# Kernel optimization log

Hardware: AMD Instinct MI355X
Metric: run time of the kernel (lower is better)

## Reference

```python
import jax, jax.numpy as jnp
import numpy as np
import math

V_ORDER = 22
N_ORDER = 22
HID = 128
MAX_ABS = 0.99
LOG_F0_MIN = math.log(80.0)
LOG_F0_MAX = math.log(1000.0)
OUT = 1 + V_ORDER + 1 + N_ORDER + 1 + HID  # 175


def setup_inputs() -> dict:
    key = jax.random.key(0)
    k1, k2, k3 = jax.random.split(key, 3)
    B, F, D = 32, 1000, 1024
    h = jax.random.normal(k1, (B, F, D), jnp.float32)
    W = jax.random.normal(k2, (OUT, D), jnp.float32) * 0.02
    b = jax.random.normal(k3, (OUT,), jnp.float32) * 0.1
    return {"h": h, "W": W, "b": b}


def _logits2biquads(logits):
    # conj representation: logits (..., 2) -> monic biquad coeffs (..., 3)
    mag = jax.nn.sigmoid(logits[..., 0]) * MAX_ABS
    phase = jax.nn.sigmoid(logits[..., 1]) * jnp.pi
    a1 = -2.0 * mag * jnp.cos(phase)
    a2 = mag * mag
    return jnp.stack([jnp.ones_like(a1), a1, a2], axis=-1)


def _biquads2lpc(biquads):
    # biquads: (..., S, 3) monic sections -> full LPC poly coeffs (..., 2S)
    # sequentially convolve the S second-order sections (b0 == 1 exactly)
    S = biquads.shape[-2]
    L = 2 * S + 1
    poly = jnp.zeros(biquads.shape[:-2] + (L,), biquads.dtype).at[..., 0].set(1.0)

    def shift(p, n):
        pad = [(0, 0)] * (p.ndim - 1) + [(n, 0)]
        return jnp.pad(p, pad)[..., :L]

    for i in range(S):  # small fixed S (=11), fully vectorized over batch/frames
        a1 = biquads[..., i, 1:2]
        a2 = biquads[..., i, 2:3]
        poly = poly + shift(poly, 1) * a1 + shift(poly, 2) * a2
    return poly[..., 1:]  # drop leading 1


def reference(h, W, b):
    B, F, _ = h.shape
    y = jnp.einsum('bfd,od->bfo', h, W) + b  # backbone out_linear
    idx = np.cumsum([1, V_ORDER, 1, N_ORDER, 1])
    f0_l, v_lpc_l, v_gain_l, n_lpc_l, n_gain_l, h_feat = jnp.split(y, idx, axis=-1)
    f0 = jnp.exp(jax.nn.sigmoid(f0_l[..., 0]) * (LOG_F0_MAX - LOG_F0_MIN) + LOG_F0_MIN)
    voice_lpc = _biquads2lpc(_logits2biquads(v_lpc_l.reshape(B, F, -1, 2)))
    noise_lpc = _biquads2lpc(_logits2biquads(n_lpc_l.reshape(B, F, -1, 2)))
    voice_gain = jnp.exp(v_gain_l[..., 0])
    noise_gain = jnp.exp(n_gain_l[..., 0])
    # flat version of (f0, (h,), (voice_gain, voice_lpc), (noise_gain, noise_lpc), ())
    return (f0, h_feat, voice_gain, voice_lpc, noise_gain, noise_lpc)
```

## Files before the change

### kernel.cpp

```cpp
#include <hip/hip_runtime.h>
#include <math.h>

#define D_DIM  1024
#define OUT_N  175
#define HID_N  128
#define BM     64
#define BK     32
#define NWR    176
#define LDK    40

#define V_OFF   1
#define VG_OFF  23
#define N_OFF   24
#define NG_OFF  46
#define HF_OFF  47

#define LOG_F0_MIN 4.3820266346738812f
#define LOG_F0_MAX 6.9077552789821368f
#define PI_F       3.14159265358979323846f

typedef __attribute__((ext_vector_type(8))) short s16x8;
typedef __attribute__((ext_vector_type(4))) short s16x4;
typedef __attribute__((ext_vector_type(4))) float f32x4;

static __device__ __forceinline__ short f2bf(float f) {
    unsigned u = __float_as_uint(f);
    unsigned r = (u + 0x7fffu + ((u >> 16) & 1u)) >> 16;
    return (short)r;
}
static __device__ __forceinline__ float bf2f(short s) {
    return __uint_as_float(((unsigned)(unsigned short)s) << 16);
}

__global__ __launch_bounds__(256) void split_w_kernel(
    const float* __restrict__ W, short* __restrict__ whi, short* __restrict__ wlo)
{
    const int n = blockIdx.x;
    const int k = threadIdx.x << 2;
    float4 v = make_float4(0.f, 0.f, 0.f, 0.f);
    if (n < OUT_N) v = *(const float4*)(W + (size_t)n * D_DIM + k);
    s16x4 hv, lv;
    hv.x = f2bf(v.x); lv.x = f2bf(v.x - bf2f(hv.x));
    hv.y = f2bf(v.y); lv.y = f2bf(v.y - bf2f(hv.y));
    hv.z = f2bf(v.z); lv.z = f2bf(v.z - bf2f(hv.z));
    hv.w = f2bf(v.w); lv.w = f2bf(v.w - bf2f(hv.w));
    *(s16x4*)(whi + n * D_DIM + k) = hv;
    *(s16x4*)(wlo + n * D_DIM + k) = lv;
}

#define SMEM_BYTES 45312

__global__ __launch_bounds__(256) void glottal_main(
    const float* __restrict__ h, const short* __restrict__ whi,
    const short* __restrict__ wlo, const float* __restrict__ bias,
    float* __restrict__ out, int R)
{
    __shared__ __align__(16) char smem[SMEM_BYTES];
    short* AhiS = (short*)smem;
    short* AloS = AhiS + BM * LDK;
    short* WhiS = AloS + BM * LDK;
    short* WloS = WhiS + NWR * LDK;
    float (*yS)[OUT_N + 2] = (float (*)[OUT_N + 2])smem;

    const int tid = threadIdx.x;
    const int r0  = blockIdx.x * BM;

    const int rA  = tid >> 3;
    const int kqA = (tid & 7) << 2;
    const int rW  = tid >> 2;
    const int kqW = (tid & 3) << 3;

    const int lane = tid & 63;
    const int wid  = tid >> 6;
    const int c    = lane & 15;
    const int kg   = lane >> 4;
    const int jcnt = (wid < 3) ? 3 : 2;
    const int fragOff = c * LDK + kg * 8;

    f32x4 acc[4][3];
    #pragma unroll
    for (int m = 0; m < 4; ++m)
        #pragma unroll
        for (int jj = 0; jj < 3; ++jj) acc[m][jj] = f32x4{0.f, 0.f, 0.f, 0.f};

    float4 apf0, apf1;
    s16x8 wph0, wph1, wph2, wpl0, wpl1, wpl2;

    int gA0 = r0 + rA;      if (gA0 >= R) gA0 = R - 1;
    int gA1 = r0 + rA + 32; if (gA1 >= R) gA1 = R - 1;
    const float* hP0 = h + (size_t)gA0 * D_DIM + kqA;
    const float* hP1 = h + (size_t)gA1 * D_DIM + kqA;
    const int nW0 = rW, nW1 = rW + 64, nW2 = rW + 128;
    const short* wHP = whi + rW * D_DIM + kqW;
    const short* wLP = wlo + rW * D_DIM + kqW;
    const bool w2ok = (nW2 < NWR);

    apf0 = *(const float4*)(hP0);
    apf1 = *(const float4*)(hP1);
    wph0 = *(const s16x8*)(wHP);
    wpl0 = *(const s16x8*)(wLP);
    wph1 = *(const s16x8*)(wHP + 64 * D_DIM);
    wpl1 = *(const s16x8*)(wLP + 64 * D_DIM);
    if (w2ok) { wph2 = *(const s16x8*)(wHP + 128 * D_DIM);
                wpl2 = *(const s16x8*)(wLP + 128 * D_DIM); }

    for (int kt = 0; kt < D_DIM; kt += BK) {
        {
            s16x4 hv, lv;
            hv.x = f2bf(apf0.x); lv.x = f2bf(apf0.x - bf2f(hv.x));
            hv.y = f2bf(apf0.y); lv.y = f2bf(apf0.y - bf2f(hv.y));
            hv.z = f2bf(apf0.z); lv.z = f2bf(apf0.z - bf2f(hv.z));
            hv.w = f2bf(apf0.w); lv.w = f2bf(apf0.w - bf2f(hv.w));
            *(s16x4*)(AhiS + rA * LDK + kqA) = hv;
            *(s16x4*)(AloS + rA * LDK + kqA) = lv;
            hv.x = f2bf(apf1.x); lv.x = f2bf(apf1.x - bf2f(hv.x));
            hv.y = f2bf(apf1.y); lv.y = f2bf(apf1.y - bf2f(hv.y));
            hv.z = f2bf(apf1.z); lv.z = f2bf(apf1.z - bf2f(hv.z));
            hv.w = f2bf(apf1.w); lv.w = f2bf(apf1.w - bf2f(hv.w));
            *(s16x4*)(AhiS + (rA + 32) * LDK + kqA) = hv;
            *(s16x4*)(AloS + (rA + 32) * LDK + kqA) = lv;
            *(s16x8*)(WhiS + nW0 * LDK + kqW) = wph0;
            *(s16x8*)(WloS + nW0 * LDK + kqW) = wpl0;
            *(s16x8*)(WhiS + nW1 * LDK + kqW) = wph1;
            *(s16x8*)(WloS + nW1 * LDK + kqW) = wpl1;
            if (w2ok) {
                *(s16x8*)(WhiS + nW2 * LDK + kqW) = wph2;
                *(s16x8*)(WloS + nW2 * LDK + kqW) = wpl2;
            }
        }
        __syncthreads();

        const int ktn = kt + BK;
        if (ktn < D_DIM) {
            apf0 = *(const float4*)(hP0 + ktn);
            apf1 = *(const float4*)(hP1 + ktn);
            wph0 = *(const s16x8*)(wHP + ktn);
            wpl0 = *(const s16x8*)(wLP + ktn);
            wph1 = *(const s16x8*)(wHP + 64 * D_DIM + ktn);
            wpl1 = *(const s16x8*)(wLP + 64 * D_DIM + ktn);
            if (w2ok) { wph2 = *(const s16x8*)(wHP + 128 * D_DIM + ktn);
                        wpl2 = *(const s16x8*)(wLP + 128 * D_DIM + ktn); }
        }

        s16x8 ahv[4], alv[4];
        #pragma unroll
        for (int m = 0; m < 4; ++m) {
            ahv[m] = *(const s16x8*)(AhiS + (m << 4) * LDK + fragOff);
            alv[m] = *(const s16x8*)(AloS + (m << 4) * LDK + fragOff);
        }
        #pragma unroll
        for (int jj = 0; jj < 3; ++jj) {
            if (jj < jcnt) {
                const int j = wid * 3 + jj;
                s16x8 bh = *(const s16x8*)(WhiS + (j << 4) * LDK + fragOff);
                s16x8 bl = *(const s16x8*)(WloS + (j << 4) * LDK + fragOff);
                #pragma unroll
                for (int m = 0; m < 4; ++m) {
                    acc[m][jj] = __builtin_amdgcn_mfma_f32_16x16x32_bf16(ahv[m], bh, acc[m][jj], 0, 0, 0);
                    acc[m][jj] = __builtin_amdgcn_mfma_f32_16x16x32_bf16(ahv[m], bl, acc[m][jj], 0, 0, 0);
                    acc[m][jj] = __builtin_amdgcn_mfma_f32_16x16x32_bf16(alv[m], bh, acc[m][jj], 0, 0, 0);
                }
            }
        }
        __syncthreads();
    }

    #pragma unroll
    for (int jj = 0; jj < 3; ++jj) {
        if (jj < jcnt) {
            const int j   = wid * 3 + jj;
            const int col = (j << 4) + c;
            if (col < OUT_N) {
                const float bb = bias[col];
                #pragma unroll
                for (int m = 0; m < 4; ++m)
                    #pragma unroll
                    for (int r = 0; r < 4; ++r)
                        yS[(m << 4) + (kg << 2) + r][col] = acc[m][jj][r] + bb;
            }
        }
    }
    __syncthreads();

    const size_t Rz = (size_t)R;

    for (int e = tid; e < BM * HID_N; e += 256) {
        int rr = e >> 7, cc = e & (HID_N - 1);
        int gr = r0 + rr;
        if (gr < R)
            out[Rz + (size_t)gr * HID_N + cc] = yS[rr][HF_OFF + cc];
    }

    if (tid < 2 * BM) {
        const int rr   = tid >> 1;
        const int half = tid & 1;
        const int gr   = r0 + rr;
        if (gr < R) {
            const float* yrow = yS[rr];

            if (half == 0) {
                float s = 1.f / (1.f + expf(-yrow[0]));
                out[gr] = expf(s * (LOG_F0_MAX - LOG_F0_MIN) + LOG_F0_MIN);
            }

            const int lbase = half ? N_OFF  : V_OFF;
            const int gidx  = half ? NG_OFF : VG_OFF;
            float*    gout  = out + (half ? Rz * 152 : Rz * 129);
            float*    lout  = out + (half ? Rz * 153 : Rz * 130);

            gout[gr] = expf(yrow[gidx]);

            float poly[23];
            poly[0] = 1.f;
            #pragma unroll
            for (int j = 1; j < 23; ++j) poly[j] = 0.f;

            #pragma unroll
            for (int i = 0; i < 11; ++i) {
                float l0  = yrow[lbase + 2 * i];
                float l1  = yrow[lbase + 2 * i + 1];
                float mag = 0.99f / (1.f + expf(-l0));
                float ph  = PI_F   / (1.f + expf(-l1));
                float a1  = -2.f * mag * cosf(ph);
                float a2  = mag * mag;
                #pragma unroll
                for (int j = 22; j >= 2; --j)
                    poly[j] = fmaf(a1, poly[j - 1], fmaf(a2, poly[j - 2], poly[j]));
                poly[1] = fmaf(a1, poly[0], poly[1]);
            }

            #pragma unroll
            for (int j = 0; j < 22; ++j)
                lout[(size_t)gr * 22 + j] = poly[j + 1];
        }
    }
}

extern "C" void kernel_launch(void* const* d_in, const int* in_sizes, int n_in,
                              void* d_out, int out_size, void* d_ws, size_t ws_size,
                              hipStream_t stream) {
    const float* h    = (const float*)d_in[0];
    const float* W    = (const float*)d_in[1];
    const float* bias = (const float*)d_in[2];
    float* out        = (float*)d_out;

    const int R = in_sizes[0] / D_DIM;
    const int blocks = (R + BM - 1) / BM;

    short* whi = (short*)d_ws;
    short* wlo = whi + NWR * D_DIM;

    split_w_kernel<<<NWR, 256, 0, stream>>>(W, whi, wlo);
    glottal_main<<<blocks, 256, 0, stream>>>(h, whi, wlo, bias, out, R);
}
```

Baseline: 216.7 us.

## Pre-swizzle W into MFMA fragment layout and load B directly from global

The weight split kernel now writes W hi/lo parts in per-lane MFMA fragment order, so the main kernel reads B operands straight from global/L2 into registers instead of staging them through LDS. The main kernel grows to 512 threads arranged as 2 row-halves by 4 column groups, and LDS shrinks to the A tile only, which should allow higher occupancy and fewer LDS writes and barriers' worth of traffic. The hidden-feature columns are written directly from the accumulators, and only the first 47 columns go through LDS for the LPC epilogue. The risk is that each wave now issues more global loads per k-step, so performance depends on L2 hit rate for W, and the direct hidden-feature stores are less coalesced.

```diff
diff --git a/kernel.cpp b/kernel.cpp
--- a/kernel.cpp
+++ b/kernel.cpp
@@ -6,8 +6,10 @@
 #define HID_N  128
 #define BM     64
 #define BK     32
-#define NWR    176
+#define NT     (D_DIM / BK)
 #define LDK    40
+#define NFRAG  11
+#define FRAG_STRIDE 512
 
 #define V_OFF   1
 #define VG_OFF  23
@@ -32,164 +34,167 @@
     return __uint_as_float(((unsigned)(unsigned short)s) << 16);
 }
 
-__global__ __launch_bounds__(256) void split_w_kernel(
-    const float* __restrict__ W, short* __restrict__ whi, short* __restrict__ wlo)
+__global__ __launch_bounds__(64) void build_wfrag(
+    const float* __restrict__ W, short* __restrict__ whiF, short* __restrict__ wloF)
 {
-    const int n = blockIdx.x;
-    const int k = threadIdx.x << 2;
-    float4 v = make_float4(0.f, 0.f, 0.f, 0.f);
-    if (n < OUT_N) v = *(const float4*)(W + (size_t)n * D_DIM + k);
-    s16x4 hv, lv;
-    hv.x = f2bf(v.x); lv.x = f2bf(v.x - bf2f(hv.x));
-    hv.y = f2bf(v.y); lv.y = f2bf(v.y - bf2f(hv.y));
-    hv.z = f2bf(v.z); lv.z = f2bf(v.z - bf2f(hv.z));
-    hv.w = f2bf(v.w); lv.w = f2bf(v.w - bf2f(hv.w));
-    *(s16x4*)(whi + n * D_DIM + k) = hv;
-    *(s16x4*)(wlo + n * D_DIM + k) = lv;
-}
-
-#define SMEM_BYTES 45312
-
-__global__ __launch_bounds__(256) void glottal_main(
-    const float* __restrict__ h, const short* __restrict__ whi,
-    const short* __restrict__ wlo, const float* __restrict__ bias,
+    const int ft   = blockIdx.x;
+    const int j    = ft >> 5;
+    const int t    = ft & 31;
+    const int lane = threadIdx.x;
+    const int n    = 16 * j + (lane & 15);
+    const int k    = 32 * t + (lane >> 4) * 8;
+
+    float v[8];
+    if (n < OUT_N) {
+        float4 p0 = *(const float4*)(W + (size_t)n * D_DIM + k);
+        float4 p1 = *(const float4*)(W + (size_t)n * D_DIM + k + 4);
+        v[0] = p0.x; v[1] = p0.y; v[2] = p0.z; v[3] = p0.w;
+        v[4] = p1.x; v[5] = p1.y; v[6] = p1.z; v[7] = p1.w;
+    } else {
+        #pragma unroll
+        for (int e = 0; e < 8; ++e) v[e] = 0.f;
+    }
+    s16x8 hv, lv;
+    #pragma unroll
+    for (int e = 0; e < 8; ++e) {
+        short hb = f2bf(v[e]);
+        hv[e] = hb;
+        lv[e] = f2bf(v[e] - bf2f(hb));
+    }
+    const size_t off = ((size_t)ft * 64 + lane) * 8;
+    *(s16x8*)(whiF + off) = hv;
+    *(s16x8*)(wloF + off) = lv;
+}
+
+#define SMEM_BYTES 12544
+
+__global__ __launch_bounds__(512, 4) void glottal_main(
+    const float* __restrict__ h, const short* __restrict__ whiF,
+    const short* __restrict__ wloF, const float* __restrict__ bias,
     float* __restrict__ out, int R)
 {
     __shared__ __align__(16) char smem[SMEM_BYTES];
     short* AhiS = (short*)smem;
     short* AloS = AhiS + BM * LDK;
-    short* WhiS = AloS + BM * LDK;
-    short* WloS = WhiS + NWR * LDK;
-    float (*yS)[OUT_N + 2] = (float (*)[OUT_N + 2])smem;
-
-    const int tid = threadIdx.x;
-    const int r0  = blockIdx.x * BM;
-
-    const int rA  = tid >> 3;
-    const int kqA = (tid & 7) << 2;
-    const int rW  = tid >> 2;
-    const int kqW = (tid & 3) << 3;
+    float (*yS)[49] = (float (*)[49])smem;
+
+    const int tid  = threadIdx.x;
+    const int r0   = blockIdx.x * BM;
 
     const int lane = tid & 63;
     const int wid  = tid >> 6;
     const int c    = lane & 15;
     const int kg   = lane >> 4;
-    const int jcnt = (wid < 3) ? 3 : 2;
-    const int fragOff = c * LDK + kg * 8;
-
-    f32x4 acc[4][3];
-    #pragma unroll
-    for (int m = 0; m < 4; ++m)
-        #pragma unroll
-        for (int jj = 0; jj < 3; ++jj) acc[m][jj] = f32x4{0.f, 0.f, 0.f, 0.f};
-
-    float4 apf0, apf1;
-    s16x8 wph0, wph1, wph2, wpl0, wpl1, wpl2;
-
-    int gA0 = r0 + rA;      if (gA0 >= R) gA0 = R - 1;
-    int gA1 = r0 + rA + 32; if (gA1 >= R) gA1 = R - 1;
-    const float* hP0 = h + (size_t)gA0 * D_DIM + kqA;
-    const float* hP1 = h + (size_t)gA1 * D_DIM + kqA;
-    const int nW0 = rW, nW1 = rW + 64, nW2 = rW + 128;
-    const short* wHP = whi + rW * D_DIM + kqW;
-    const short* wLP = wlo + rW * D_DIM + kqW;
-    const bool w2ok = (nW2 < NWR);
-
-    apf0 = *(const float4*)(hP0);
-    apf1 = *(const float4*)(hP1);
-    wph0 = *(const s16x8*)(wHP);
-    wpl0 = *(const s16x8*)(wLP);
-    wph1 = *(const s16x8*)(wHP + 64 * D_DIM);
-    wpl1 = *(const s16x8*)(wLP + 64 * D_DIM);
-    if (w2ok) { wph2 = *(const s16x8*)(wHP + 128 * D_DIM);
-                wpl2 = *(const s16x8*)(wLP + 128 * D_DIM); }
-
-    for (int kt = 0; kt < D_DIM; kt += BK) {
+    const int mh   = wid >> 2;
+    const int jg   = wid & 3;
+    const int jcnt = (jg < 3) ? 3 : 2;
+
+    const int rA  = tid >> 3;
+    const int kqA = (tid & 7) << 2;
+    int gA = r0 + rA; if (gA >= R) gA = R - 1;
+    const float* hP = h + (size_t)gA * D_DIM + kqA;
+
+    const short* bhP[3];
+    const short* blP[3];
+    #pragma unroll
+    for (int jj = 0; jj < 3; ++jj) {
+        int j = 3 * jg + jj; if (j > NFRAG - 1) j = NFRAG - 1;
+        bhP[jj] = whiF + (size_t)j * NT * FRAG_STRIDE + lane * 8;
+        blP[jj] = wloF + (size_t)j * NT * FRAG_STRIDE + lane * 8;
+    }
+
+    f32x4 acc[2][3];
+    #pragma unroll
+    for (int mm = 0; mm < 2; ++mm)
+        #pragma unroll
+        for (int jj = 0; jj < 3; ++jj) acc[mm][jj] = f32x4{0.f, 0.f, 0.f, 0.f};
+
+    float4 aC = *(const float4*)(hP);
+    s16x8 bhC[3], blC[3];
+    #pragma unroll
+    for (int jj = 0; jj < 3; ++jj) if (jj < jcnt) {
+        bhC[jj] = *(const s16x8*)(bhP[jj]);
+        blC[jj] = *(const s16x8*)(blP[jj]);
+    }
+
+    for (int t = 0; t < NT; ++t) {
         {
             s16x4 hv, lv;
-            hv.x = f2bf(apf0.x); lv.x = f2bf(apf0.x - bf2f(hv.x));
-            hv.y = f2bf(apf0.y); lv.y = f2bf(apf0.y - bf2f(hv.y));
-            hv.z = f2bf(apf0.z); lv.z = f2bf(apf0.z - bf2f(hv.z));
-            hv.w = f2bf(apf0.w); lv.w = f2bf(apf0.w - bf2f(hv.w));
+            hv.x = f2bf(aC.x); lv.x = f2bf(aC.x - bf2f(hv.x));
+            hv.y = f2bf(aC.y); lv.y = f2bf(aC.y - bf2f(hv.y));
+            hv.z = f2bf(aC.z); lv.z = f2bf(aC.z - bf2f(hv.z));
+            hv.w = f2bf(aC.w); lv.w = f2bf(aC.w - bf2f(hv.w));
             *(s16x4*)(AhiS + rA * LDK + kqA) = hv;
             *(s16x4*)(AloS + rA * LDK + kqA) = lv;
-            hv.x = f2bf(apf1.x); lv.x = f2bf(apf1.x - bf2f(hv.x));
-            hv.y = f2bf(apf1.y); lv.y = f2bf(apf1.y - bf2f(hv.y));
-            hv.z = f2bf(apf1.z); lv.z = f2bf(apf1.z - bf2f(hv.z));
-            hv.w = f2bf(apf1.w); lv.w = f2bf(apf1.w - bf2f(hv.w));
-            *(s16x4*)(AhiS + (rA + 32) * LDK + kqA) = hv;
-            *(s16x4*)(AloS + (rA + 32) * LDK + kqA) = lv;
-            *(s16x8*)(WhiS + nW0 * LDK + kqW) = wph0;
-            *(s16x8*)(WloS + nW0 * LDK + kqW) = wpl0;
-            *(s16x8*)(WhiS + nW1 * LDK + kqW) = wph1;
-            *(s16x8*)(WloS + nW1 * LDK + kqW) = wpl1;
-            if (w2ok) {
-                *(s16x8*)(WhiS + nW2 * LDK + kqW) = wph2;
-                *(s16x8*)(WloS + nW2 * LDK + kqW) = wpl2;
-            }
         }
         __syncthreads();
 
-        const int ktn = kt + BK;
-        if (ktn < D_DIM) {
-            apf0 = *(const float4*)(hP0 + ktn);
-            apf1 = *(const float4*)(hP1 + ktn);
-            wph0 = *(const s16x8*)(wHP + ktn);
-            wpl0 = *(const s16x8*)(wLP + ktn);
-            wph1 = *(const s16x8*)(wHP + 64 * D_DIM + ktn);
-            wpl1 = *(const s16x8*)(wLP + 64 * D_DIM + ktn);
-            if (w2ok) { wph2 = *(const s16x8*)(wHP + 128 * D_DIM + ktn);
-                        wpl2 = *(const s16x8*)(wLP + 128 * D_DIM + ktn); }
-        }
-
-        s16x8 ahv[4], alv[4];
-        #pragma unroll
-        for (int m = 0; m < 4; ++m) {
-            ahv[m] = *(const s16x8*)(AhiS + (m << 4) * LDK + fragOff);
-            alv[m] = *(const s16x8*)(AloS + (m << 4) * LDK + fragOff);
-        }
-        #pragma unroll
-        for (int jj = 0; jj < 3; ++jj) {
-            if (jj < jcnt) {
-                const int j = wid * 3 + jj;
-                s16x8 bh = *(const s16x8*)(WhiS + (j << 4) * LDK + fragOff);
-                s16x8 bl = *(const s16x8*)(WloS + (j << 4) * LDK + fragOff);
+        float4 aN;
+        s16x8 bhN[3], blN[3];
+        const bool more = (t + 1 < NT);
+        if (more) {
+            aN = *(const float4*)(hP + (t + 1) * BK);
+            #pragma unroll
+            for (int jj = 0; jj < 3; ++jj) if (jj < jcnt) {
+                bhN[jj] = *(const s16x8*)(bhP[jj] + (size_t)(t + 1) * FRAG_STRIDE);
+                blN[jj] = *(const s16x8*)(blP[jj] + (size_t)(t + 1) * FRAG_STRIDE);
+            }
+        }
+
+        s16x8 ah[2], al[2];
+        #pragma unroll
+        for (int mm = 0; mm < 2; ++mm) {
+            const int ro = (32 * mh + 16 * mm + c) * LDK + kg * 8;
+            ah[mm] = *(const s16x8*)(AhiS + ro);
+            al[mm] = *(const s16x8*)(AloS + ro);
+        }
+
+        #pragma unroll
+        for (int jj = 0; jj < 3; ++jj) if (jj < jcnt) {
+            #pragma unroll
+            for (int mm = 0; mm < 2; ++mm) {
+                acc[mm][jj] = __builtin_amdgcn_mfma_f32_16x16x32_bf16(ah[mm], bhC[jj], acc[mm][jj], 0, 0, 0);
+                acc[mm][jj] = __builtin_amdgcn_mfma_f32_16x16x32_bf16(ah[mm], blC[jj], acc[mm][jj], 0, 0, 0);
+                acc[mm][jj] = __builtin_amdgcn_mfma_f32_16x16x32_bf16(al[mm], bhC[jj], acc[mm][jj], 0, 0, 0);
+            }
+        }
+        __syncthreads();
+
+        if (more) {
+            aC = aN;
+            #pragma unroll
+            for (int jj = 0; jj < 3; ++jj) if (jj < jcnt) {
+                bhC[jj] = bhN[jj];
+                blC[jj] = blN[jj];
+            }
+        }
+    }
+
+    const size_t Rz = (size_t)R;
+
+    #pragma unroll
+    for (int jj = 0; jj < 3; ++jj) if (jj < jcnt) {
+        const int j   = 3 * jg + jj;
+        const int col = 16 * j + c;
+        const float bb = (col < OUT_N) ? bias[col] : 0.f;
+        #pragma unroll
+        for (int mm = 0; mm < 2; ++mm) {
+            const int rb = 32 * mh + 16 * mm + (kg << 2);
+            if (col >= HF_OFF && col < OUT_N) {
                 #pragma unroll
-                for (int m = 0; m < 4; ++m) {
-                    acc[m][jj] = __builtin_amdgcn_mfma_f32_16x16x32_bf16(ahv[m], bh, acc[m][jj], 0, 0, 0);
-                    acc[m][jj] = __builtin_amdgcn_mfma_f32_16x16x32_bf16(ahv[m], bl, acc[m][jj], 0, 0, 0);
-                    acc[m][jj] = __builtin_amdgcn_mfma_f32_16x16x32_bf16(alv[m], bh, acc[m][jj], 0, 0, 0);
+                for (int r = 0; r < 4; ++r) {
+                    int gr = r0 + rb + r;
+                    if (gr < R)
+                        out[Rz + (size_t)gr * HID_N + (col - HF_OFF)] = acc[mm][jj][r] + bb;
                 }
-            }
-        }
-        __syncthreads();
-    }
-
-    #pragma unroll
-    for (int jj = 0; jj < 3; ++jj) {
-        if (jj < jcnt) {
-            const int j   = wid * 3 + jj;
-            const int col = (j << 4) + c;
-            if (col < OUT_N) {
-                const float bb = bias[col];
+            } else if (col < HF_OFF) {
                 #pragma unroll
-                for (int m = 0; m < 4; ++m)
-                    #pragma unroll
-                    for (int r = 0; r < 4; ++r)
-                        yS[(m << 4) + (kg << 2) + r][col] = acc[m][jj][r] + bb;
+                for (int r = 0; r < 4; ++r)
+                    yS[rb + r][col] = acc[mm][jj][r] + bb;
             }
         }
     }
     __syncthreads();
-
-    const size_t Rz = (size_t)R;
-
-    for (int e = tid; e < BM * HID_N; e += 256) {
-        int rr = e >> 7, cc = e & (HID_N - 1);
-        int gr = r0 + rr;
-        if (gr < R)
-            out[Rz + (size_t)gr * HID_N + cc] = yS[rr][HF_OFF + cc];
-    }
 
     if (tid < 2 * BM) {
         const int rr   = tid >> 1;
@@ -247,9 +252,9 @@
     const int R = in_sizes[0] / D_DIM;
     const int blocks = (R + BM - 1) / BM;
 
-    short* whi = (short*)d_ws;
-    short* wlo = whi + NWR * D_DIM;
-
-    split_w_kernel<<<NWR, 256, 0, stream>>>(W, whi, wlo);
-    glottal_main<<<blocks, 256, 0, stream>>>(h, whi, wlo, bias, out, R);
-}
+    short* whiF = (short*)d_ws;
+    short* wloF = whiF + (size_t)NFRAG * NT * FRAG_STRIDE;
+
+    build_wfrag<<<NFRAG * NT, 64, 0, stream>>>(W, whiF, wloF);
+    glottal_main<<<blocks, 512, 0, stream>>>(h, whiF, wloF, bias, out, R);
+}
```

Measured after the change: 226.2 us. +4.4%, slower.
